# Optimization experiments

Measured on AMD Instinct MI355X. Metric: run time of the kernel, lower is better.

## Reference

```python
import jax, jax.numpy as jnp
import numpy as np

N = 50000   # nodes
E = 800000  # edges (avg degree 16)
D = 128     # input feature dim
H = 128     # hidden_units per FFN layer
BN_EPS = 1e-3  # keras BatchNormalization default epsilon


def setup_inputs() -> dict:
    key = jax.random.key(0)
    ks = jax.random.split(key, 16)
    inp = {}
    inp["node_repr"] = jax.random.normal(ks[0], (N, D), dtype=jnp.float32)
    inp["edges"] = jax.random.randint(ks[1], (2, E), 0, N, dtype=jnp.int32)
    inp["edge_weights"] = jnp.ones((E,), jnp.float32)
    idx = 2
    # ffn_prepare: D -> H -> H ; update_fn: (D+H) -> H -> H
    for pre, dims in [("prep", [(D, H), (H, H)]), ("upd", [(D + H, H), (H, H)])]:
        for li, (din, dout) in enumerate(dims):
            inp[f"{pre}_bn{li}_g"] = jnp.ones((din,), jnp.float32)
            inp[f"{pre}_bn{li}_b"] = jnp.zeros((din,), jnp.float32)
            inp[f"{pre}_bn{li}_m"] = jax.random.normal(ks[idx], (din,), dtype=jnp.float32) * 0.1; idx += 1
            inp[f"{pre}_bn{li}_v"] = jnp.ones((din,), jnp.float32)
            inp[f"{pre}_W{li}"] = jax.random.normal(ks[idx], (din, dout), dtype=jnp.float32) * (din ** -0.5); idx += 1
            inp[f"{pre}_b{li}"] = jnp.zeros((dout,), jnp.float32)
    return inp


def _ffn(x, layers):
    # layers: list of (bn_gamma, bn_beta, bn_mean, bn_var, W, b)
    # each block: BatchNorm (inference) -> Dropout (identity at eval) -> Dense+gelu
    for g, b, m, v, W, bias in layers:
        x = (x - m) * jax.lax.rsqrt(v + BN_EPS) * g + b
        x = jax.nn.gelu(x @ W + bias, approximate=False)
    return x


def reference(node_repr, edges, edge_weights,
              prep_bn0_g, prep_bn0_b, prep_bn0_m, prep_bn0_v, prep_W0, prep_b0,
              prep_bn1_g, prep_bn1_b, prep_bn1_m, prep_bn1_v, prep_W1, prep_b1,
              upd_bn0_g, upd_bn0_b, upd_bn0_m, upd_bn0_v, upd_W0, upd_b0,
              upd_bn1_g, upd_bn1_b, upd_bn1_m, upd_bn1_v, upd_W1, upd_b1):
    node_indices, neighbour_indices = edges[0], edges[1]
    # prepare: gather neighbours, per-edge FFN, scale by edge weight
    nbr = jnp.take(node_repr, neighbour_indices, axis=0)  # [E, D]
    prep_layers = [(prep_bn0_g, prep_bn0_b, prep_bn0_m, prep_bn0_v, prep_W0, prep_b0),
                   (prep_bn1_g, prep_bn1_b, prep_bn1_m, prep_bn1_v, prep_W1, prep_b1)]
    messages = _ffn(nbr, prep_layers) * edge_weights[:, None]  # [E, H]
    # aggregate: unsorted_segment_mean (empty segments -> 0, as in TF)
    ssum = jax.ops.segment_sum(messages, node_indices, num_segments=node_repr.shape[0])
    cnt = jax.ops.segment_sum(jnp.ones((messages.shape[0],), messages.dtype), node_indices,
                              num_segments=node_repr.shape[0])
    agg = jnp.where(cnt[:, None] > 0, ssum / jnp.maximum(cnt, 1.0)[:, None], 0.0)  # [N, H]
    # update: concat + FFN
    h = jnp.concatenate([node_repr, agg], axis=1)  # [N, D+H]
    upd_layers = [(upd_bn0_g, upd_bn0_b, upd_bn0_m, upd_bn0_v, upd_W0, upd_b0),
                  (upd_bn1_g, upd_bn1_b, upd_bn1_m, upd_bn1_v, upd_W1, upd_b1)]
    return _ffn(h, upd_layers)  # [N, H]
```

## Files before the change

kernel.cpp:

```cpp
#include <hip/hip_runtime.h>
#include <math.h>

#define NN 50000
#define NE 800000
#define DD 128
#define HH 128
#define BN_EPS 1e-3f
#define PBLK 1563
#define EBLK 3125
#define WBLK 512
#define PGRID 512
#define MAXD 64

typedef _Float16 f16x8 __attribute__((ext_vector_type(8)));
typedef float f32x4 __attribute__((ext_vector_type(4)));

#define PIN(v) asm volatile("" : : "v"(v))

__device__ __forceinline__ float gelu_f(float x) {
    float t = x * (1.5957691f + 0.07135481f * x * x);
    float e = __expf(-t);
    return x * __builtin_amdgcn_rcpf(1.0f + e);
}

struct WArgs {
    const float *W, *g, *bb, *m, *v, *bias;
    _Float16* wt; float* bs; int K;
};

__global__ __launch_bounds__(256)
void wdeg_kernel(WArgs a0, WArgs a1, WArgs a2, WArgs a3,
                 const int* __restrict__ edges, int* __restrict__ deg,
                 int* __restrict__ pos)
{
    if (blockIdx.x >= WBLK) {
        int e = (blockIdx.x - WBLK) * 256 + threadIdx.x;
        if (e < NE) pos[e] = atomicAdd(&deg[edges[e]], 1);
        return;
    }
    __shared__ float red[256];
    const int which = blockIdx.x >> 7;
    const int n = blockIdx.x & 127;
    WArgs a = a0;
    if (which == 1) a = a1;
    else if (which == 2) a = a2;
    else if (which == 3) a = a3;
    const int t = threadIdx.x;
    float part = 0.0f;
    for (int k = t; k < a.K; k += 256) {
        float sc = a.g[k] * rsqrtf(a.v[k] + BN_EPS);
        float sh = a.bb[k] - a.m[k] * sc;
        float wv = a.W[(long long)k * HH + n];
        a.wt[(long long)n * a.K + k] = (_Float16)(wv * sc);
        part += sh * wv;
    }
    red[t] = part;
    __syncthreads();
    for (int s = 128; s > 0; s >>= 1) {
        if (t < s) red[t] += red[t + s];
        __syncthreads();
    }
    if (t == 0) a.bs[n] = a.bias[n] + red[0];
}

__global__ __launch_bounds__(256, 2)
void prep_fill_kernel(const float* __restrict__ x,
                      const _Float16* __restrict__ wt0, const float* __restrict__ bs0,
                      const _Float16* __restrict__ wt1, const float* __restrict__ bs1,
                      _Float16* __restrict__ msg,
                      const int* __restrict__ edges, const float* __restrict__ ew,
                      const int* __restrict__ pos, int2* __restrict__ rec)
{
    __shared__ __align__(16) _Float16 ys[32 * HH];
    if (blockIdx.x >= PGRID) {
        int e = (blockIdx.x - PGRID) * 256 + threadIdx.x;
        if (e < NE) {
            int d = edges[e];
            int p = pos[e];
            if (p < MAXD) {
                int2 r;
                r.x = edges[NE + e];
                r.y = __float_as_int(ew[e]);
                rec[(long long)d * MAXD + p] = r;
            }
        }
        return;
    }
    const int tid = threadIdx.x;
    const int w = tid >> 6, lane = tid & 63;
    const int cl = lane & 15;
    const int kg = lane >> 4;

    f16x8 b0[4][2], b1[4][2];
#pragma unroll
    for (int kc = 0; kc < 4; ++kc)
#pragma unroll
        for (int ct = 0; ct < 2; ++ct) {
            int col = w * 32 + ct * 16 + cl;
            b0[kc][ct] = *reinterpret_cast<const f16x8*>(&wt0[(long long)col * DD + kc * 32 + kg * 8]);
            b1[kc][ct] = *reinterpret_cast<const f16x8*>(&wt1[(long long)col * HH + kc * 32 + kg * 8]);
        }
#pragma unroll
    for (int kc = 0; kc < 4; ++kc) { PIN(b0[kc][0]); PIN(b0[kc][1]); PIN(b1[kc][0]); PIN(b1[kc][1]); }

    const f32x4 zero = {0.0f, 0.0f, 0.0f, 0.0f};

    for (int tile = blockIdx.x; tile < PBLK; tile += PGRID) {
        const int row0 = tile * 32;

        f32x4 acc[2][2];
#pragma unroll
        for (int rt = 0; rt < 2; ++rt)
#pragma unroll
            for (int ct = 0; ct < 2; ++ct) acc[rt][ct] = zero;

#pragma unroll
        for (int kc = 0; kc < 4; ++kc) {
#pragma unroll
            for (int rt = 0; rt < 2; ++rt) {
                int row = row0 + rt * 16 + cl;
                if (row >= NN) row = NN - 1;
                const float4* p = reinterpret_cast<const float4*>(&x[(long long)row * DD + kc * 32 + kg * 8]);
                float4 u0 = p[0], u1 = p[1];
                f16x8 a;
                a[0] = (_Float16)u0.x; a[1] = (_Float16)u0.y; a[2] = (_Float16)u0.z; a[3] = (_Float16)u0.w;
                a[4] = (_Float16)u1.x; a[5] = (_Float16)u1.y; a[6] = (_Float16)u1.z; a[7] = (_Float16)u1.w;
#pragma unroll
                for (int ct = 0; ct < 2; ++ct)
                    acc[rt][ct] = __builtin_amdgcn_mfma_f32_16x16x32_f16(a, b0[kc][ct], acc[rt][ct], 0, 0, 0);
            }
        }

#pragma unroll
        for (int ct = 0; ct < 2; ++ct) {
            int col = w * 32 + ct * 16 + cl;
            float bias = bs0[col];
#pragma unroll
            for (int rt = 0; rt < 2; ++rt)
#pragma unroll
                for (int rr = 0; rr < 4; ++rr) {
                    int r = rt * 16 + kg * 4 + rr;
                    float vv = gelu_f(acc[rt][ct][rr] + bias);
                    int slot = (r * 16 + (col >> 3)) ^ (r & 7);
                    ys[slot * 8 + (col & 7)] = (_Float16)vv;
                }
        }
        __syncthreads();

        f32x4 acc2[2][2];
#pragma unroll
        for (int rt = 0; rt < 2; ++rt)
#pragma unroll
            for (int ct = 0; ct < 2; ++ct) acc2[rt][ct] = zero;

#pragma unroll
        for (int kc = 0; kc < 4; ++kc) {
            int k8 = kc * 4 + kg;
#pragma unroll
            for (int rt = 0; rt < 2; ++rt) {
                int rA = rt * 16 + cl;
                int slot = (rA * 16 + k8) ^ (rA & 7);
                f16x8 a = *reinterpret_cast<const f16x8*>(&ys[slot * 8]);
#pragma unroll
                for (int ct = 0; ct < 2; ++ct)
                    acc2[rt][ct] = __builtin_amdgcn_mfma_f32_16x16x32_f16(a, b1[kc][ct], acc2[rt][ct], 0, 0, 0);
            }
        }

#pragma unroll
        for (int ct = 0; ct < 2; ++ct) {
            int col = w * 32 + ct * 16 + cl;
            float bias = bs1[col];
#pragma unroll
            for (int rt = 0; rt < 2; ++rt)
#pragma unroll
                for (int rr = 0; rr < 4; ++rr) {
                    int row = row0 + rt * 16 + kg * 4 + rr;
                    if (row < NN)
                        msg[(long long)row * HH + col] = (_Float16)gelu_f(acc2[rt][ct][rr] + bias);
                }
        }
        __syncthreads();
    }
}

__global__ __launch_bounds__(256)
void gather_kernel(const int* __restrict__ deg, const int2* __restrict__ rec,
                   const _Float16* __restrict__ msg, _Float16* __restrict__ aggh)
{
    int gwave = (blockIdx.x * 256 + threadIdx.x) >> 6;
    int lane = threadIdx.x & 63;
    int sub = lane >> 4, l16 = lane & 15;
    int node = gwave * 4 + sub;
    if (node >= NN) return;
    int d = deg[node];
    if (d > MAXD) d = MAXD;
    long long beg = (long long)node * MAXD;
    float acc[8];
#pragma unroll
    for (int q = 0; q < 8; ++q) acc[q] = 0.0f;
    for (int j = 0; j < d; ++j) {
        int2 rc = rec[beg + j];
        int src = rc.x;
        float w = __int_as_float(rc.y);
        f16x8 m = *reinterpret_cast<const f16x8*>(&msg[(long long)src * HH + l16 * 8]);
#pragma unroll
        for (int q = 0; q < 8; ++q) acc[q] += (float)m[q] * w;
    }
    float inv = (d > 0) ? 1.0f / (float)d : 0.0f;
    f16x8 o;
#pragma unroll
    for (int q = 0; q < 8; ++q) o[q] = (_Float16)(acc[q] * inv);
    *reinterpret_cast<f16x8*>(&aggh[(long long)node * HH + l16 * 8]) = o;
}

__global__ __launch_bounds__(256, 2)
void upd_kernel(const float* __restrict__ x, const _Float16* __restrict__ aggh,
                const _Float16* __restrict__ wt2, const float* __restrict__ bs2,
                const _Float16* __restrict__ wt3, const float* __restrict__ bs3,
                float* __restrict__ out)
{
    __shared__ __align__(16) _Float16 ys[32 * HH];
    const int tid = threadIdx.x;
    const int w = tid >> 6, lane = tid & 63;
    const int cl = lane & 15;
    const int kg = lane >> 4;

    f16x8 b0[8][2], b1[4][2];
#pragma unroll
    for (int kc = 0; kc < 8; ++kc)
#pragma unroll
        for (int ct = 0; ct < 2; ++ct) {
            int col = w * 32 + ct * 16 + cl;
            b0[kc][ct] = *reinterpret_cast<const f16x8*>(&wt2[(long long)col * 256 + kc * 32 + kg * 8]);
        }
#pragma unroll
    for (int kc = 0; kc < 4; ++kc)
#pragma unroll
        for (int ct = 0; ct < 2; ++ct) {
            int col = w * 32 + ct * 16 + cl;
            b1[kc][ct] = *reinterpret_cast<const f16x8*>(&wt3[(long long)col * HH + kc * 32 + kg * 8]);
        }
#pragma unroll
    for (int kc = 0; kc < 4; ++kc) { PIN(b0[kc][0]); PIN(b0[kc][1]); PIN(b1[kc][0]); PIN(b1[kc][1]); }
#pragma unroll
    for (int kc = 4; kc < 8; ++kc) { PIN(b0[kc][0]); PIN(b0[kc][1]); }

    const f32x4 zero = {0.0f, 0.0f, 0.0f, 0.0f};

    for (int tile = blockIdx.x; tile < PBLK; tile += PGRID) {
        const int row0 = tile * 32;

        f32x4 acc[2][2];
#pragma unroll
        for (int rt = 0; rt < 2; ++rt)
#pragma unroll
            for (int ct = 0; ct < 2; ++ct) acc[rt][ct] = zero;

#pragma unroll
        for (int kc = 0; kc < 8; ++kc) {
#pragma unroll
            for (int rt = 0; rt < 2; ++rt) {
                int row = row0 + rt * 16 + cl;
                if (row >= NN) row = NN - 1;
                f16x8 a;
                if (kc < 4) {
                    const float4* p = reinterpret_cast<const float4*>(&x[(long long)row * DD + kc * 32 + kg * 8]);
                    float4 u0 = p[0], u1 = p[1];
                    a[0] = (_Float16)u0.x; a[1] = (_Float16)u0.y; a[2] = (_Float16)u0.z; a[3] = (_Float16)u0.w;
                    a[4] = (_Float16)u1.x; a[5] = (_Float16)u1.y; a[6] = (_Float16)u1.z; a[7] = (_Float16)u1.w;
                } else {
                    a = *reinterpret_cast<const f16x8*>(&aggh[(long long)row * HH + (kc - 4) * 32 + kg * 8]);
                }
#pragma unroll
                for (int ct = 0; ct < 2; ++ct)
                    acc[rt][ct] = __builtin_amdgcn_mfma_f32_16x16x32_f16(a, b0[kc][ct], acc[rt][ct], 0, 0, 0);
            }
        }

#pragma unroll
        for (int ct = 0; ct < 2; ++ct) {
            int col = w * 32 + ct * 16 + cl;
            float bias = bs2[col];
#pragma unroll
            for (int rt = 0; rt < 2; ++rt)
#pragma unroll
                for (int rr = 0; rr < 4; ++rr) {
                    int r = rt * 16 + kg * 4 + rr;
                    float vv = gelu_f(acc[rt][ct][rr] + bias);
                    int slot = (r * 16 + (col >> 3)) ^ (r & 7);
                    ys[slot * 8 + (col & 7)] = (_Float16)vv;
                }
        }
        __syncthreads();

        f32x4 acc2[2][2];
#pragma unroll
        for (int rt = 0; rt < 2; ++rt)
#pragma unroll
            for (int ct = 0; ct < 2; ++ct) acc2[rt][ct] = zero;

#pragma unroll
        for (int kc = 0; kc < 4; ++kc) {
            int k8 = kc * 4 + kg;
#pragma unroll
            for (int rt = 0; rt < 2; ++rt) {
                int rA = rt * 16 + cl;
                int slot = (rA * 16 + k8) ^ (rA & 7);
                f16x8 a = *reinterpret_cast<const f16x8*>(&ys[slot * 8]);
#pragma unroll
                for (int ct = 0; ct < 2; ++ct)
                    acc2[rt][ct] = __builtin_amdgcn_mfma_f32_16x16x32_f16(a, b1[kc][ct], acc2[rt][ct], 0, 0, 0);
            }
        }

#pragma unroll
        for (int ct = 0; ct < 2; ++ct) {
            int col = w * 32 + ct * 16 + cl;
            float bias = bs3[col];
#pragma unroll
            for (int rt = 0; rt < 2; ++rt)
#pragma unroll
                for (int rr = 0; rr < 4; ++rr) {
                    int row = row0 + rt * 16 + kg * 4 + rr;
                    if (row < NN)
                        out[(long long)row * HH + col] = gelu_f(acc2[rt][ct][rr] + bias);
                }
        }
        __syncthreads();
    }
}

extern "C" void kernel_launch(void* const* d_in, const int* in_sizes, int n_in,
                              void* d_out, int out_size, void* d_ws, size_t ws_size,
                              hipStream_t stream) {
    const float* node_repr = (const float*)d_in[0];
    const int*   edges     = (const int*)d_in[1];
    const float* ew        = (const float*)d_in[2];

    const float* prep_bn0_g = (const float*)d_in[3];
    const float* prep_bn0_b = (const float*)d_in[4];
    const float* prep_bn0_m = (const float*)d_in[5];
    const float* prep_bn0_v = (const float*)d_in[6];
    const float* prep_W0    = (const float*)d_in[7];
    const float* prep_b0    = (const float*)d_in[8];
    const float* prep_bn1_g = (const float*)d_in[9];
    const float* prep_bn1_b = (const float*)d_in[10];
    const float* prep_bn1_m = (const float*)d_in[11];
    const float* prep_bn1_v = (const float*)d_in[12];
    const float* prep_W1    = (const float*)d_in[13];
    const float* prep_b1    = (const float*)d_in[14];

    const float* upd_bn0_g = (const float*)d_in[15];
    const float* upd_bn0_b = (const float*)d_in[16];
    const float* upd_bn0_m = (const float*)d_in[17];
    const float* upd_bn0_v = (const float*)d_in[18];
    const float* upd_W0    = (const float*)d_in[19];
    const float* upd_b0    = (const float*)d_in[20];
    const float* upd_bn1_g = (const float*)d_in[21];
    const float* upd_bn1_b = (const float*)d_in[22];
    const float* upd_bn1_m = (const float*)d_in[23];
    const float* upd_bn1_v = (const float*)d_in[24];
    const float* upd_W1    = (const float*)d_in[25];
    const float* upd_b1    = (const float*)d_in[26];

    _Float16* msg  = (_Float16*)d_ws;
    _Float16* aggh = msg + (size_t)NN * HH;
    _Float16* wt0  = aggh + (size_t)NN * HH;
    _Float16* wt1  = wt0 + 128 * 128;
    _Float16* wt2  = wt1 + 128 * 128;
    _Float16* wt3  = wt2 + 128 * 256;
    float* bs0 = (float*)(wt3 + 128 * 128);
    float* bs1 = bs0 + 128;
    float* bs2 = bs1 + 128;
    float* bs3 = bs2 + 128;
    int* deg    = (int*)(bs3 + 128);
    int* pos    = deg + NN;
    int2* rec   = (int2*)(pos + NE);

    hipMemsetAsync(deg, 0, (size_t)NN * sizeof(int), stream);

    WArgs a0 = {prep_W0, prep_bn0_g, prep_bn0_b, prep_bn0_m, prep_bn0_v, prep_b0, wt0, bs0, DD};
    WArgs a1 = {prep_W1, prep_bn1_g, prep_bn1_b, prep_bn1_m, prep_bn1_v, prep_b1, wt1, bs1, HH};
    WArgs a2 = {upd_W0, upd_bn0_g, upd_bn0_b, upd_bn0_m, upd_bn0_v, upd_b0, wt2, bs2, DD + HH};
    WArgs a3 = {upd_W1, upd_bn1_g, upd_bn1_b, upd_bn1_m, upd_bn1_v, upd_b1, wt3, bs3, HH};

    wdeg_kernel<<<WBLK + EBLK, 256, 0, stream>>>(a0, a1, a2, a3, edges, deg, pos);

    prep_fill_kernel<<<PGRID + EBLK, 256, 0, stream>>>(node_repr, wt0, bs0, wt1, bs1,
                                                       msg, edges, ew, pos, rec);

    int gblk = (NN + 15) / 16;
    gather_kernel<<<gblk, 256, 0, stream>>>(deg, rec, msg, aggh);

    upd_kernel<<<PGRID, 256, 0, stream>>>(node_repr, aggh, wt2, bs2, wt3, bs3,
                                          (float*)d_out);
}
```

Baseline: 151.0 us.

## Fuse degree counting into bucket fill and raise occupancy of GEMM kernels

Edge degree counting via atomicAdd moves from the weight-prep kernel into the bucket-fill blocks of the prep kernel, so the pos array and its extra write/read pass over all edges go away. The mean divisor now uses the uncapped degree. Occupancy hints rise for the prep (2→4) and update (2→3) kernels, and their grids grow to 1024 and 768 blocks. Higher occupancy may force register spills of the pinned weight fragments.

```diff
diff --git a/kernel.cpp b/kernel.cpp
--- a/kernel.cpp
+++ b/kernel.cpp
@@ -8,8 +8,8 @@
 #define BN_EPS 1e-3f
 #define PBLK 1563
 #define EBLK 3125
-#define WBLK 512
-#define PGRID 512
+#define PGRID 1024
+#define UGRID 768
 #define MAXD 64
 
 typedef _Float16 f16x8 __attribute__((ext_vector_type(8)));
@@ -29,15 +29,8 @@
 };
 
 __global__ __launch_bounds__(256)
-void wdeg_kernel(WArgs a0, WArgs a1, WArgs a2, WArgs a3,
-                 const int* __restrict__ edges, int* __restrict__ deg,
-                 int* __restrict__ pos)
+void weights_kernel(WArgs a0, WArgs a1, WArgs a2, WArgs a3)
 {
-    if (blockIdx.x >= WBLK) {
-        int e = (blockIdx.x - WBLK) * 256 + threadIdx.x;
-        if (e < NE) pos[e] = atomicAdd(&deg[edges[e]], 1);
-        return;
-    }
     __shared__ float red[256];
     const int which = blockIdx.x >> 7;
     const int n = blockIdx.x & 127;
@@ -63,20 +56,20 @@
     if (t == 0) a.bs[n] = a.bias[n] + red[0];
 }
 
-__global__ __launch_bounds__(256, 2)
+__global__ __launch_bounds__(256, 4)
 void prep_fill_kernel(const float* __restrict__ x,
                       const _Float16* __restrict__ wt0, const float* __restrict__ bs0,
                       const _Float16* __restrict__ wt1, const float* __restrict__ bs1,
                       _Float16* __restrict__ msg,
                       const int* __restrict__ edges, const float* __restrict__ ew,
-                      const int* __restrict__ pos, int2* __restrict__ rec)
+                      int* __restrict__ deg, int2* __restrict__ rec)
 {
     __shared__ __align__(16) _Float16 ys[32 * HH];
     if (blockIdx.x >= PGRID) {
         int e = (blockIdx.x - PGRID) * 256 + threadIdx.x;
         if (e < NE) {
             int d = edges[e];
-            int p = pos[e];
+            int p = atomicAdd(&deg[d], 1);
             if (p < MAXD) {
                 int2 r;
                 r.x = edges[NE + e];
@@ -193,8 +186,8 @@
     int sub = lane >> 4, l16 = lane & 15;
     int node = gwave * 4 + sub;
     if (node >= NN) return;
-    int d = deg[node];
-    if (d > MAXD) d = MAXD;
+    int dfull = deg[node];
+    int d = (dfull > MAXD) ? MAXD : dfull;
     long long beg = (long long)node * MAXD;
     float acc[8];
 #pragma unroll
@@ -207,14 +200,14 @@
 #pragma unroll
         for (int q = 0; q < 8; ++q) acc[q] += (float)m[q] * w;
     }
-    float inv = (d > 0) ? 1.0f / (float)d : 0.0f;
+    float inv = (dfull > 0) ? 1.0f / (float)dfull : 0.0f;
     f16x8 o;
 #pragma unroll
     for (int q = 0; q < 8; ++q) o[q] = (_Float16)(acc[q] * inv);
     *reinterpret_cast<f16x8*>(&aggh[(long long)node * HH + l16 * 8]) = o;
 }
 
-__global__ __launch_bounds__(256, 2)
+__global__ __launch_bounds__(256, 3)
 void upd_kernel(const float* __restrict__ x, const _Float16* __restrict__ aggh,
                 const _Float16* __restrict__ wt2, const float* __restrict__ bs2,
                 const _Float16* __restrict__ wt3, const float* __restrict__ bs3,
@@ -248,7 +241,7 @@
 
     const f32x4 zero = {0.0f, 0.0f, 0.0f, 0.0f};
 
-    for (int tile = blockIdx.x; tile < PBLK; tile += PGRID) {
+    for (int tile = blockIdx.x; tile < PBLK; tile += UGRID) {
         const int row0 = tile * 32;
 
         f32x4 acc[2][2];
@@ -375,8 +368,7 @@
     float* bs2 = bs1 + 128;
     float* bs3 = bs2 + 128;
     int* deg    = (int*)(bs3 + 128);
-    int* pos    = deg + NN;
-    int2* rec   = (int2*)(pos + NE);
+    int2* rec   = (int2*)(deg + NN + 2);
 
     hipMemsetAsync(deg, 0, (size_t)NN * sizeof(int), stream);
 
@@ -385,14 +377,14 @@
     WArgs a2 = {upd_W0, upd_bn0_g, upd_bn0_b, upd_bn0_m, upd_bn0_v, upd_b0, wt2, bs2, DD + HH};
     WArgs a3 = {upd_W1, upd_bn1_g, upd_bn1_b, upd_bn1_m, upd_bn1_v, upd_b1, wt3, bs3, HH};
 
-    wdeg_kernel<<<WBLK + EBLK, 256, 0, stream>>>(a0, a1, a2, a3, edges, deg, pos);
+    weights_kernel<<<512, 256, 0, stream>>>(a0, a1, a2, a3);
 
     prep_fill_kernel<<<PGRID + EBLK, 256, 0, stream>>>(node_repr, wt0, bs0, wt1, bs1,
-                                                       msg, edges, ew, pos, rec);
+                                                       msg, edges, ew, deg, rec);
 
     int gblk = (NN + 15) / 16;
     gather_kernel<<<gblk, 256, 0, stream>>>(deg, rec, msg, aggh);
 
-    upd_kernel<<<PGRID, 256, 0, stream>>>(node_repr, aggh, wt2, bs2, wt3, bs3,
+    upd_kernel<<<UGRID, 256, 0, stream>>>(node_repr, aggh, wt2, bs2, wt3, bs3,
                                           (float*)d_out);
 }
```

Measured after the change: 166.5 us. 1.1x slower.
